# Optimization experiments

Measured on AMD Instinct MI355X. Metric: run time of the kernel, lower is better.

Reference implementation:

```python
import jax, jax.numpy as jnp
import numpy as np

MIN_DISTANCE = 1.0  # default forward arg of the torch module


def setup_inputs() -> dict:
    key = jax.random.key(0)
    k1, k2 = jax.random.split(key)
    B, N = 4, 4096
    coords = jax.random.normal(k1, (B, N, 3), dtype=jnp.float32) * 5.0
    steric_radii = jax.random.uniform(k2, (B, N), dtype=jnp.float32)
    return {"coords": coords, "steric_radii": steric_radii}


def reference(coords, steric_radii):
    # coords: [B,N,3], steric_radii: [B,N]
    diff = coords[:, :, None, :] - coords[:, None, :, :]          # [B,N,N,3]
    d2 = jnp.sum(diff * diff, axis=-1)                             # [B,N,N]
    # safe sqrt: exact 0 on the diagonal (matches torch.cdist), no NaN grads
    pairwise = jnp.where(d2 > 0, jnp.sqrt(jnp.where(d2 > 0, d2, 1.0)), 0.0)
    sr = steric_radii[:, :, None] + steric_radii[:, None, :]       # [B,N,N]
    target = jnp.maximum(MIN_DISTANCE, sr)
    penalty = jax.nn.relu(target - pairwise)[..., None]            # [B,N,N,1]
    direction = jnp.clip(diff, -1.0, 1.0)                          # [B,N,N,3]
    adjustment = jnp.mean(penalty * direction, axis=2)             # [B,N,3]
    return coords + 0.1 * adjustment
```

## Files before the change

kernel.cpp:

```cpp
#include <hip/hip_runtime.h>

#define BB 4
#define NN 4096
#define TI 256
#define JB 32
#define JLEN (NN / JB)
#define GRP 8

#if __has_builtin(__builtin_amdgcn_sqrtf)
  #define FAST_SQRT __builtin_amdgcn_sqrtf
#else
  #define FAST_SQRT sqrtf
#endif

__device__ __forceinline__ float clip1(float x) {
    return fminf(fmaxf(x, -1.0f), 1.0f);
}

#define PACK_ELEMS (BB * NN)
#define PART_OFF   (PACK_ELEMS * 4)

__global__ __launch_bounds__(256) void ncp_pack(
    const float* __restrict__ coords,
    const float* __restrict__ radii,
    float4* __restrict__ packed)
{
    const int t = blockIdx.x * 256 + threadIdx.x;
    if (t >= PACK_ELEMS) return;
    packed[t] = make_float4(coords[t * 3 + 0], coords[t * 3 + 1],
                            coords[t * 3 + 2], radii[t]);
}

__global__ __launch_bounds__(TI) void ncp_partial(
    const float4* __restrict__ packed,
    float* __restrict__ part)
{
    const int b = blockIdx.z;
    const int i = blockIdx.x * TI + threadIdx.x;
    const int s = blockIdx.y;
    const float4* jsrc = packed + b * NN + s * JLEN;

    const float4 me = packed[b * NN + i];
    const float xi = me.x, yi = me.y, zi = me.z, ri = me.w;

    float ax = 0.0f, ay = 0.0f, az = 0.0f;

    for (int k0 = 0; k0 < JLEN; k0 += GRP) {
        float dx[GRP], dy[GRP], dz[GRP], d2[GRP], rj[GRP];
        #pragma unroll
        for (int u = 0; u < GRP; ++u) {
            const float4 c = jsrc[k0 + u];
            dx[u] = xi - c.x;
            dy[u] = yi - c.y;
            dz[u] = zi - c.z;
            d2[u] = fmaf(dx[u], dx[u], fmaf(dy[u], dy[u], dz[u] * dz[u]));
            rj[u] = c.w;
        }
        #pragma unroll
        for (int u = 0; u < GRP; ++u) {
            if (__any(d2[u] < 4.0f)) {
                const float dist = FAST_SQRT(d2[u]);
                const float tgt = fmaxf(1.0f, ri + rj[u]);
                const float p = fmaxf(tgt - dist, 0.0f);
                ax = fmaf(p, clip1(dx[u]), ax);
                ay = fmaf(p, clip1(dy[u]), ay);
                az = fmaf(p, clip1(dz[u]), az);
            }
        }
    }

    float* dst = part + (size_t)s * (BB * NN * 3);
    const int o = (b * NN + i) * 3;
    dst[o + 0] = ax;
    dst[o + 1] = ay;
    dst[o + 2] = az;
}

__global__ __launch_bounds__(256) void ncp_reduce(
    const float* __restrict__ coords,
    const float* __restrict__ part,
    float* __restrict__ out)
{
    const int o = blockIdx.x * 256 + threadIdx.x;
    if (o >= BB * NN * 3) return;
    float acc = 0.0f;
    #pragma unroll
    for (int s = 0; s < JB; ++s)
        acc += part[(size_t)s * (BB * NN * 3) + o];
    out[o] = fmaf(0.1f / (float)NN, acc, coords[o]);
}

__global__ __launch_bounds__(TI) void ncp_direct(
    const float* __restrict__ coords,
    const float* __restrict__ radii,
    float* __restrict__ out)
{
    __shared__ float4 jt[TI];
    const int b = blockIdx.z;
    const int i = blockIdx.x * TI + threadIdx.x;

    const float xi = coords[(b * NN + i) * 3 + 0];
    const float yi = coords[(b * NN + i) * 3 + 1];
    const float zi = coords[(b * NN + i) * 3 + 2];
    const float ri = radii[b * NN + i];

    float ax = 0.0f, ay = 0.0f, az = 0.0f;

    for (int jc = 0; jc < NN; jc += TI) {
        const int jj = jc + threadIdx.x;
        __syncthreads();
        jt[threadIdx.x] = make_float4(coords[(b * NN + jj) * 3 + 0],
                                      coords[(b * NN + jj) * 3 + 1],
                                      coords[(b * NN + jj) * 3 + 2],
                                      radii[b * NN + jj]);
        __syncthreads();
        #pragma unroll 4
        for (int k = 0; k < TI; ++k) {
            const float4 c = jt[k];
            const float dx = xi - c.x;
            const float dy = yi - c.y;
            const float dz = zi - c.z;
            const float d2 = fmaf(dx, dx, fmaf(dy, dy, dz * dz));
            if (__any(d2 < 4.0f)) {
                const float dist = FAST_SQRT(d2);
                const float tgt = fmaxf(1.0f, ri + c.w);
                const float p = fmaxf(tgt - dist, 0.0f);
                ax = fmaf(p, clip1(dx), ax);
                ay = fmaf(p, clip1(dy), ay);
                az = fmaf(p, clip1(dz), az);
            }
        }
    }

    const int o = (b * NN + i) * 3;
    const float sc = 0.1f / (float)NN;
    out[o + 0] = fmaf(sc, ax, coords[o + 0]);
    out[o + 1] = fmaf(sc, ay, coords[o + 1]);
    out[o + 2] = fmaf(sc, az, coords[o + 2]);
}

extern "C" void kernel_launch(void* const* d_in, const int* in_sizes, int n_in,
                              void* d_out, int out_size, void* d_ws, size_t ws_size,
                              hipStream_t stream) {
    const float* coords = (const float*)d_in[0];
    const float* radii  = (const float*)d_in[1];
    float* out = (float*)d_out;
    const int n = BB * NN * 3;
    const size_t need = (size_t)(PART_OFF + (size_t)JB * n) * sizeof(float);

    if (ws_size >= need) {
        float4* packed = (float4*)d_ws;
        float* part = (float*)d_ws + PART_OFF;
        ncp_pack<<<(PACK_ELEMS + 255) / 256, 256, 0, stream>>>(coords, radii, packed);
        ncp_partial<<<dim3(NN / TI, JB, BB), TI, 0, stream>>>(packed, part);
        ncp_reduce<<<(n + 255) / 256, 256, 0, stream>>>(coords, part, out);
    } else {
        ncp_direct<<<dim3(NN / TI, 1, BB), TI, 0, stream>>>(coords, radii, out);
    }
}
```

Measured before the change: 79.74 us.

## Use norm-expansion distance test with register-blocked multiple i per thread

The partial kernel now has each thread own four i points. The distance screen is rewritten as |xj|^2 - 2 xi·xj compared against 4 - |xi|^2, which costs three FMAs per pair and uses squared norms precomputed in the pack kernel. The j range is split into 128 slices instead of 32, and the partial-sum layout becomes component-major so stores and reduce loads are coalesced. This cuts per-pair ALU work on the common far-pair path and reuses each j load across four i points. In exchange the reduction reads four times more partial data, and the expanded form can lose precision when deciding near-threshold pairs.

```diff
diff --git a/kernel.cpp b/kernel.cpp
--- a/kernel.cpp
+++ b/kernel.cpp
@@ -3,9 +3,10 @@
 #define BB 4
 #define NN 4096
 #define TI 256
-#define JB 32
+#define IPT 4
+#define JB 128
 #define JLEN (NN / JB)
-#define GRP 8
+#define GRP 2
 
 #if __has_builtin(__builtin_amdgcn_sqrtf)
   #define FAST_SQRT __builtin_amdgcn_sqrtf
@@ -18,62 +19,94 @@
 }
 
 #define PACK_ELEMS (BB * NN)
-#define PART_OFF   (PACK_ELEMS * 4)
+#define N2_OFF   (PACK_ELEMS * 4)
+#define PART_OFF (N2_OFF + PACK_ELEMS)
 
 __global__ __launch_bounds__(256) void ncp_pack(
     const float* __restrict__ coords,
     const float* __restrict__ radii,
-    float4* __restrict__ packed)
+    float4* __restrict__ p4,
+    float* __restrict__ n2a)
 {
     const int t = blockIdx.x * 256 + threadIdx.x;
     if (t >= PACK_ELEMS) return;
-    packed[t] = make_float4(coords[t * 3 + 0], coords[t * 3 + 1],
-                            coords[t * 3 + 2], radii[t]);
+    const float x = coords[t * 3 + 0];
+    const float y = coords[t * 3 + 1];
+    const float z = coords[t * 3 + 2];
+    p4[t] = make_float4(x, y, z, radii[t]);
+    n2a[t] = fmaf(z, z, fmaf(y, y, x * x));
 }
 
-__global__ __launch_bounds__(TI) void ncp_partial(
-    const float4* __restrict__ packed,
+__global__ __launch_bounds__(TI, 8) void ncp_partial(
+    const float4* __restrict__ p4,
+    const float* __restrict__ n2a,
     float* __restrict__ part)
 {
     const int b = blockIdx.z;
-    const int i = blockIdx.x * TI + threadIdx.x;
     const int s = blockIdx.y;
-    const float4* jsrc = packed + b * NN + s * JLEN;
+    const int i0 = blockIdx.x * (TI * IPT) + threadIdx.x;
 
-    const float4 me = packed[b * NN + i];
-    const float xi = me.x, yi = me.y, zi = me.z, ri = me.w;
+    float m2x[IPT], m2y[IPT], m2z[IPT], thr[IPT], ri[IPT];
+    float ax[IPT], ay[IPT], az[IPT];
+    #pragma unroll
+    for (int u = 0; u < IPT; ++u) {
+        const int i = i0 + u * TI;
+        const float4 me = p4[b * NN + i];
+        m2x[u] = -2.0f * me.x;
+        m2y[u] = -2.0f * me.y;
+        m2z[u] = -2.0f * me.z;
+        ri[u]  = me.w;
+        thr[u] = 4.0f - n2a[b * NN + i];
+        ax[u] = 0.0f; ay[u] = 0.0f; az[u] = 0.0f;
+    }
 
-    float ax = 0.0f, ay = 0.0f, az = 0.0f;
+    const float4* jp = p4  + b * NN + s * JLEN;
+    const float*  jn = n2a + b * NN + s * JLEN;
 
     for (int k0 = 0; k0 < JLEN; k0 += GRP) {
-        float dx[GRP], dy[GRP], dz[GRP], d2[GRP], rj[GRP];
+        float4 c[GRP];
+        float  nj[GRP];
+        float  sd[GRP][IPT];
         #pragma unroll
-        for (int u = 0; u < GRP; ++u) {
-            const float4 c = jsrc[k0 + u];
-            dx[u] = xi - c.x;
-            dy[u] = yi - c.y;
-            dz[u] = zi - c.z;
-            d2[u] = fmaf(dx[u], dx[u], fmaf(dy[u], dy[u], dz[u] * dz[u]));
-            rj[u] = c.w;
+        for (int g = 0; g < GRP; ++g) {
+            c[g]  = jp[k0 + g];
+            nj[g] = jn[k0 + g];
         }
         #pragma unroll
-        for (int u = 0; u < GRP; ++u) {
-            if (__any(d2[u] < 4.0f)) {
-                const float dist = FAST_SQRT(d2[u]);
-                const float tgt = fmaxf(1.0f, ri + rj[u]);
-                const float p = fmaxf(tgt - dist, 0.0f);
-                ax = fmaf(p, clip1(dx[u]), ax);
-                ay = fmaf(p, clip1(dy[u]), ay);
-                az = fmaf(p, clip1(dz[u]), az);
+        for (int g = 0; g < GRP; ++g)
+            #pragma unroll
+            for (int u = 0; u < IPT; ++u)
+                sd[g][u] = fmaf(m2z[u], c[g].z,
+                           fmaf(m2y[u], c[g].y,
+                           fmaf(m2x[u], c[g].x, nj[g])));
+        #pragma unroll
+        for (int g = 0; g < GRP; ++g) {
+            #pragma unroll
+            for (int u = 0; u < IPT; ++u) {
+                if (__any(sd[g][u] < thr[u])) {
+                    const float d2   = fmaxf(sd[g][u] + (4.0f - thr[u]), 0.0f);
+                    const float dist = FAST_SQRT(d2);
+                    const float tgt  = fmaxf(1.0f, ri[u] + c[g].w);
+                    const float p    = fmaxf(tgt - dist, 0.0f);
+                    const float dx   = fmaf(-0.5f, m2x[u], -c[g].x);
+                    const float dy   = fmaf(-0.5f, m2y[u], -c[g].y);
+                    const float dz   = fmaf(-0.5f, m2z[u], -c[g].z);
+                    ax[u] = fmaf(p, clip1(dx), ax[u]);
+                    ay[u] = fmaf(p, clip1(dy), ay[u]);
+                    az[u] = fmaf(p, clip1(dz), az[u]);
+                }
             }
         }
     }
 
-    float* dst = part + (size_t)s * (BB * NN * 3);
-    const int o = (b * NN + i) * 3;
-    dst[o + 0] = ax;
-    dst[o + 1] = ay;
-    dst[o + 2] = az;
+    float* base = part + (size_t)(s * BB + b) * 3 * NN;
+    #pragma unroll
+    for (int u = 0; u < IPT; ++u) {
+        const int i = i0 + u * TI;
+        base[0 * NN + i] = ax[u];
+        base[1 * NN + i] = ay[u];
+        base[2 * NN + i] = az[u];
+    }
 }
 
 __global__ __launch_bounds__(256) void ncp_reduce(
@@ -81,12 +114,17 @@
     const float* __restrict__ part,
     float* __restrict__ out)
 {
-    const int o = blockIdx.x * 256 + threadIdx.x;
-    if (o >= BB * NN * 3) return;
+    const int t = blockIdx.x * 256 + threadIdx.x;
+    if (t >= BB * 3 * NN) return;
+    const int b = t / (3 * NN);
+    const int r = t - b * 3 * NN;
+    const int comp = r / NN;
+    const int i = r - comp * NN;
     float acc = 0.0f;
-    #pragma unroll
+    #pragma unroll 8
     for (int s = 0; s < JB; ++s)
-        acc += part[(size_t)s * (BB * NN * 3) + o];
+        acc += part[((size_t)(s * BB + b) * 3 + comp) * NN + i];
+    const int o = (b * NN + i) * 3 + comp;
     out[o] = fmaf(0.1f / (float)NN, acc, coords[o]);
 }
 
@@ -145,15 +183,16 @@
     const float* coords = (const float*)d_in[0];
     const float* radii  = (const float*)d_in[1];
     float* out = (float*)d_out;
-    const int n = BB * NN * 3;
-    const size_t need = (size_t)(PART_OFF + (size_t)JB * n) * sizeof(float);
+    const size_t part_floats = (size_t)JB * BB * 3 * NN;
+    const size_t need = (PART_OFF + part_floats) * sizeof(float);
 
     if (ws_size >= need) {
-        float4* packed = (float4*)d_ws;
+        float4* p4  = (float4*)d_ws;
+        float* n2a  = (float*)d_ws + N2_OFF;
         float* part = (float*)d_ws + PART_OFF;
-        ncp_pack<<<(PACK_ELEMS + 255) / 256, 256, 0, stream>>>(coords, radii, packed);
-        ncp_partial<<<dim3(NN / TI, JB, BB), TI, 0, stream>>>(packed, part);
-        ncp_reduce<<<(n + 255) / 256, 256, 0, stream>>>(coords, part, out);
+        ncp_pack<<<(PACK_ELEMS + 255) / 256, 256, 0, stream>>>(coords, radii, p4, n2a);
+        ncp_partial<<<dim3(NN / (TI * IPT), JB, BB), TI, 0, stream>>>(p4, n2a, part);
+        ncp_reduce<<<(BB * 3 * NN + 255) / 256, 256, 0, stream>>>(coords, part, out);
     } else {
         ncp_direct<<<dim3(NN / TI, 1, BB), TI, 0, stream>>>(coords, radii, out);
     }
```

After: 89.21 us. +11.9%, slower.
